# Kernel tuning notes

Measured on AMD Instinct MI355X. Metric: run time of the kernel, lower is better.

The kernel has to match this reference:

```python
import jax, jax.numpy as jnp
import numpy as np

B, S, D = 2, 2048, 640
H, DH = 8, 80  # heads, dim_head
SCALE = DH ** -0.5


def setup_inputs() -> dict:
    key = jax.random.key(0)
    ks = jax.random.split(key, 7)
    std = D ** -0.5
    return {
        "x": jax.random.normal(ks[0], (B, S, D), jnp.float32),
        "encoder_hidden_states": jax.random.normal(ks[1], (B, S, D), jnp.float32),
        # Linear weights stored as [in, out] so application is x @ W
        "Wq": jax.random.normal(ks[2], (D, H * DH), jnp.float32) * std,
        "Wk": jax.random.normal(ks[3], (D, H * DH), jnp.float32) * std,
        "Wv": jax.random.normal(ks[4], (D, H * DH), jnp.float32) * std,
        "Wo": jax.random.normal(ks[5], (H * DH, D), jnp.float32) * std,
        "bo": jax.random.normal(ks[6], (D,), jnp.float32) * 0.01,
    }


def reference(x, encoder_hidden_states, Wq, Wk, Wv, Wo, bo):
    # projections (to_q/to_k/to_v have bias=False)
    q = x @ Wq                      # [B, S, H*DH]
    k = encoder_hidden_states @ Wk  # [B, S, H*DH]
    v = encoder_hidden_states @ Wv  # [B, S, H*DH]

    def split_heads(t):
        b, s, _ = t.shape
        return t.reshape(b, s, H, DH).transpose(0, 2, 1, 3)  # [B, H, S, DH]

    q, k, v = split_heads(q), split_heads(k), split_heads(v)

    # the torch loop over bh-chunks computes plain softmax attention; same math fused
    scores = jnp.einsum("bhid,bhjd->bhij", q, k) * SCALE  # [B, H, Sq, Skv]
    attn = jax.nn.softmax(scores, axis=-1)
    out = jnp.einsum("bhij,bhjd->bhid", attn, v)          # [B, H, Sq, DH]

    out = out.transpose(0, 2, 1, 3).reshape(x.shape[0], x.shape[1], H * DH)
    return out @ Wo + bo  # to_out[0]; Dropout(p=0) is identity
```

## Files before the change

### kernel.cpp

```cpp
#include <hip/hip_runtime.h>
#include <hip/hip_bf16.h>

typedef __bf16 v4bf __attribute__((ext_vector_type(4)));
typedef __bf16 v8bf __attribute__((ext_vector_type(8)));
typedef float  v4f  __attribute__((ext_vector_type(4)));

namespace {
constexpr int Bb  = 2;
constexpr int Ss  = 2048;
constexpr int Dd  = 640;
constexpr int Hh  = 8;
constexpr int DHh = 80;
constexpr int Mm  = Bb * Ss;
constexpr float kQScale = 0.11180339887498949f * 1.4426950408889634f;

__device__ __forceinline__ float4 ld4(const float* p) {
  return *reinterpret_cast<const float4*>(p);
}

__device__ __forceinline__ v8bf pack8(float4 f0, float4 f1) {
  v8bf p;
  p[0]=(__bf16)f0.x; p[1]=(__bf16)f0.y; p[2]=(__bf16)f0.z; p[3]=(__bf16)f0.w;
  p[4]=(__bf16)f1.x; p[5]=(__bf16)f1.y; p[6]=(__bf16)f1.z; p[7]=(__bf16)f1.w;
  return p;
}

__device__ __forceinline__ float exp2_hw(float x) {
  float r;
  asm("v_exp_f32 %0, %1" : "=v"(r) : "v"(x));
  return r;
}
}

__global__ __launch_bounds__(256)
void wtrans_kernel(const float* __restrict__ Wq, const float* __restrict__ Wk,
                   const float* __restrict__ Wv, const float* __restrict__ Wo,
                   __bf16* __restrict__ Wtq, __bf16* __restrict__ Wtk,
                   __bf16* __restrict__ Wtv, __bf16* __restrict__ Wto) {
  const int z = blockIdx.z;
  const float* W = (z == 0) ? Wq : (z == 1) ? Wk : (z == 2) ? Wv : Wo;
  __bf16* Wt = (z == 0) ? Wtq : (z == 1) ? Wtk : (z == 2) ? Wtv : Wto;
  const int k0 = blockIdx.y * 32, n0 = blockIdx.x * 32;
  __shared__ float t[32][33];
  const int tid = threadIdx.x;
  {
    int kr = tid >> 3, c4 = (tid & 7) * 4;
    float4 f = ld4(W + (size_t)(k0 + kr) * Dd + n0 + c4);
    t[kr][c4 + 0] = f.x; t[kr][c4 + 1] = f.y;
    t[kr][c4 + 2] = f.z; t[kr][c4 + 3] = f.w;
  }
  __syncthreads();
  {
    int nr = tid >> 3, kc = (tid & 7) * 4;
    v4bf p;
#pragma unroll
    for (int u = 0; u < 4; ++u) p[u] = (__bf16)t[kc + u][nr];
    *reinterpret_cast<v4bf*>(&Wt[(size_t)(n0 + nr) * Dd + k0 + kc]) = p;
  }
}

__device__ __forceinline__ void gemm_core_db(const float* __restrict__ Af,
                                             const __bf16* __restrict__ Bt,
                                             __bf16* As, __bf16* Bs, int m0,
                                             int n0, int rh, int ch,
                                             v4f acc[4][4]) {
  constexpr int BUF = 128 * 40;
  constexpr int NKB = Dd / 32;
  const int tid = threadIdx.x;
  const int lane = tid & 63;
  const int quad = lane >> 4, l15 = lane & 15;
  const int lr = tid >> 1;
  const int lk = (tid & 1) * 16;
  const __bf16* Bg = Bt + (size_t)(n0 + lr) * Dd + lk;

#pragma unroll
  for (int i = 0; i < 4; ++i)
#pragma unroll
    for (int j = 0; j < 4; ++j) acc[i][j] = (v4f){0.f, 0.f, 0.f, 0.f};

  v8bf a0, a1, b0, b1;
  {
    const float* ap = Af + (size_t)(m0 + lr) * Dd + lk;
    a0 = pack8(ld4(ap), ld4(ap + 4));
    a1 = pack8(ld4(ap + 8), ld4(ap + 12));
  }
  b0 = *reinterpret_cast<const v8bf*>(Bg);
  b1 = *reinterpret_cast<const v8bf*>(Bg + 8);
  *reinterpret_cast<v8bf*>(&As[lr * 40 + lk])     = a0;
  *reinterpret_cast<v8bf*>(&As[lr * 40 + lk + 8]) = a1;
  *reinterpret_cast<v8bf*>(&Bs[lr * 40 + lk])     = b0;
  *reinterpret_cast<v8bf*>(&Bs[lr * 40 + lk + 8]) = b1;

  for (int it = 0; it < NKB; ++it) {
    if (it + 1 < NKB) {
      const int kb = (it + 1) * 32;
      const float* ap = Af + (size_t)(m0 + lr) * Dd + kb + lk;
      a0 = pack8(ld4(ap), ld4(ap + 4));
      a1 = pack8(ld4(ap + 8), ld4(ap + 12));
      b0 = *reinterpret_cast<const v8bf*>(Bg + kb);
      b1 = *reinterpret_cast<const v8bf*>(Bg + kb + 8);
    }
    __syncthreads();
    const int cur = (it & 1) * BUF, nxt = BUF - cur;
    v8bf af[4], bv[4];
#pragma unroll
    for (int i = 0; i < 4; ++i)
      af[i] = *reinterpret_cast<const v8bf*>(
          &As[cur + (rh + i * 16 + l15) * 40 + quad * 8]);
#pragma unroll
    for (int j = 0; j < 4; ++j)
      bv[j] = *reinterpret_cast<const v8bf*>(
          &Bs[cur + (ch + j * 16 + l15) * 40 + quad * 8]);
#pragma unroll
    for (int i = 0; i < 4; ++i)
#pragma unroll
      for (int j = 0; j < 4; ++j)
        acc[i][j] = __builtin_amdgcn_mfma_f32_16x16x32_bf16(af[i], bv[j],
                                                            acc[i][j], 0, 0, 0);
    if (it + 1 < NKB) {
      *reinterpret_cast<v8bf*>(&As[nxt + lr * 40 + lk])     = a0;
      *reinterpret_cast<v8bf*>(&As[nxt + lr * 40 + lk + 8]) = a1;
      *reinterpret_cast<v8bf*>(&Bs[nxt + lr * 40 + lk])     = b0;
      *reinterpret_cast<v8bf*>(&Bs[nxt + lr * 40 + lk + 8]) = b1;
    }
  }
}

__global__ __launch_bounds__(256)
void gemm_qkv_mfma(const float* __restrict__ x, const float* __restrict__ ehs,
                   const __bf16* __restrict__ Wtq,
                   const __bf16* __restrict__ Wtk,
                   const __bf16* __restrict__ Wtv, __bf16* __restrict__ qb,
                   __bf16* __restrict__ kbuf, __bf16* __restrict__ vb) {
  const int id = blockIdx.x;
  int z, mi, ni;
  if (id < 160) {
    int chunk = id / 40, r = id % 40;
    z = 0;
    mi = chunk * 8 + (r & 7);
    ni = r >> 3;
  } else {
    int id2 = id - 160;
    int chunk = id2 / 80, r = id2 % 80;
    int j = r >> 3;
    mi = chunk * 8 + (r & 7);
    ni = j % 5;
    z = 1 + j / 5;
  }
  const int m0 = mi * 128, n0 = ni * 128;

  const float* A = (z == 0) ? x : ehs;
  const __bf16* Bt = (z == 0) ? Wtq : (z == 1) ? Wtk : Wtv;
  __bf16* C = (z == 0) ? qb : (z == 1) ? kbuf : vb;
  const float scale = (z == 0) ? kQScale : 1.0f;

  __shared__ __bf16 As[2 * 128 * 40];
  __shared__ __bf16 Bs[2 * 128 * 40];
  const int tid = threadIdx.x;
  const int w = tid >> 6, lane = tid & 63;
  const int quad = lane >> 4, l15 = lane & 15;
  const int rh = (w >> 1) * 64, ch = (w & 1) * 64;
  v4f acc[4][4];
  gemm_core_db(A, Bt, As, Bs, m0, n0, rh, ch, acc);

  if (z == 2) {
#pragma unroll
    for (int i = 0; i < 4; ++i)
#pragma unroll
      for (int j = 0; j < 4; ++j) {
        int m = m0 + rh + i * 16 + quad * 4;
        int n = n0 + ch + j * 16 + l15;
        int hh = n / DHh, d = n % DHh;
        int bb = m >> 11, tok = m & 2047;
        int tb = tok >> 5, t = tok & 31;
        v4bf pk;
#pragma unroll
        for (int r = 0; r < 4; ++r) pk[r] = (__bf16)acc[i][j][r];
        *reinterpret_cast<v4bf*>(
            &C[((((size_t)bb * Hh + hh) * (Ss / 32) + tb) * DHh + d) * 32 +
               t]) = pk;
      }
  } else {
#pragma unroll
    for (int i = 0; i < 4; ++i)
#pragma unroll
      for (int j = 0; j < 4; ++j) {
        int m = m0 + rh + i * 16 + quad * 4;
        int n = n0 + ch + j * 16 + l15;
        int hh = n / DHh, d = n % DHh;
        int bb = m >> 11, tok = m & 2047;
        __bf16* base = &C[(((size_t)bb * Hh + hh) * Ss + tok) * DHh + d];
#pragma unroll
        for (int r = 0; r < 4; ++r)
          base[(size_t)r * DHh] = (__bf16)(acc[i][j][r] * scale);
      }
  }
}

__global__ __launch_bounds__(256)
void gemm_out_mfma(const __bf16* __restrict__ A, const __bf16* __restrict__ Bt,
                   const float* __restrict__ bias, float* __restrict__ out) {
  constexpr int BUF = 64 * 40;
  constexpr int NKB = Dd / 32;
  __shared__ __bf16 As[2 * BUF];
  __shared__ __bf16 Bs[2 * BUF];
  const int tid = threadIdx.x;
  const int w = tid >> 6, lane = tid & 63;
  const int quad = lane >> 4, l15 = lane & 15;
  const int m0 = blockIdx.y * 64, n0 = blockIdx.x * 64;
  const int rh = (w >> 1) * 32, ch = (w & 1) * 32;
  const int lr = tid >> 2, lk = (tid & 3) * 8;
  const __bf16* Ag = A + (size_t)(m0 + lr) * Dd + lk;
  const __bf16* Bg = Bt + (size_t)(n0 + lr) * Dd + lk;

  v4f acc[2][2];
#pragma unroll
  for (int i = 0; i < 2; ++i)
#pragma unroll
    for (int j = 0; j < 2; ++j) acc[i][j] = (v4f){0.f, 0.f, 0.f, 0.f};

  v8bf a0, b0;
  a0 = *reinterpret_cast<const v8bf*>(Ag);
  b0 = *reinterpret_cast<const v8bf*>(Bg);
  *reinterpret_cast<v8bf*>(&As[lr * 40 + lk]) = a0;
  *reinterpret_cast<v8bf*>(&Bs[lr * 40 + lk]) = b0;

  for (int it = 0; it < NKB; ++it) {
    if (it + 1 < NKB) {
      const int kb = (it + 1) * 32;
      a0 = *reinterpret_cast<const v8bf*>(Ag + kb);
      b0 = *reinterpret_cast<const v8bf*>(Bg + kb);
    }
    __syncthreads();
    const int cur = (it & 1) * BUF, nxt = BUF - cur;
    v8bf af[2], bv[2];
#pragma unroll
    for (int i = 0; i < 2; ++i)
      af[i] = *reinterpret_cast<const v8bf*>(
          &As[cur + (rh + i * 16 + l15) * 40 + quad * 8]);
#pragma unroll
    for (int j = 0; j < 2; ++j)
      bv[j] = *reinterpret_cast<const v8bf*>(
          &Bs[cur + (ch + j * 16 + l15) * 40 + quad * 8]);
#pragma unroll
    for (int i = 0; i < 2; ++i)
#pragma unroll
      for (int j = 0; j < 2; ++j)
        acc[i][j] = __builtin_amdgcn_mfma_f32_16x16x32_bf16(af[i], bv[j],
                                                            acc[i][j], 0, 0, 0);
    if (it + 1 < NKB) {
      *reinterpret_cast<v8bf*>(&As[nxt + lr * 40 + lk]) = a0;
      *reinterpret_cast<v8bf*>(&Bs[nxt + lr * 40 + lk]) = b0;
    }
  }

#pragma unroll
  for (int i = 0; i < 2; ++i)
#pragma unroll
    for (int j = 0; j < 2; ++j) {
      int m = m0 + rh + i * 16 + quad * 4;
      int n = n0 + ch + j * 16 + l15;
      float bn = bias[n];
#pragma unroll
      for (int r = 0; r < 4; ++r)
        out[(size_t)(m + r) * Dd + n] = acc[i][j][r] + bn;
    }
}

__global__ __launch_bounds__(256, 2)
void attn_mfma_kernel(const __bf16* __restrict__ q,
                      const __bf16* __restrict__ k,
                      const __bf16* __restrict__ vtg, __bf16* __restrict__ o) {
  constexpr int QT = 64;
  constexpr int KT = 32;
  constexpr int KW = Ss / 4;
  constexpr int NIT = KW / KT;
  constexpr int LV = 40;
  constexpr int PS = QT * LV;
  constexpr int LM = 100;

  __shared__ __align__(16) float smem_f[2 * QT * LM];

  const int bh = blockIdx.x;
  const int b = bh >> 3, h = bh & 7;
  const int q0 = blockIdx.y * QT;
  const int tid = threadIdx.x;
  const int w = tid >> 6;
  const int lane = tid & 63;
  const int quad = lane >> 4;
  const int l15 = lane & 15;

  __bf16* psw = reinterpret_cast<__bf16*>(smem_f) + w * PS;

  const __bf16* qg  = q + ((size_t)(b * Hh + h) * Ss + q0) * DHh;
  const __bf16* kgb = k + (size_t)(b * Hh + h) * Ss * DHh;
  const __bf16* vgb = vtg + (size_t)(b * Hh + h) * Ss * DHh;

  v8bf qf[4][3];
#pragma unroll
  for (int qt = 0; qt < 4; ++qt)
#pragma unroll
    for (int s = 0; s < 3; ++s) {
      if (s == 2 && quad >= 2) {
        qf[qt][s] = (v8bf){};
      } else {
        qf[qt][s] = *reinterpret_cast<const v8bf*>(
            qg + (size_t)(qt * 16 + l15) * DHh + s * 32 + quad * 8);
      }
    }

  v8bf av5 = {};
  if (l15 == 0) {
#pragma unroll
    for (int e = 0; e < 8; ++e) av5[e] = (__bf16)1.f;
  }

  v8bf kc[3][2];
#pragma unroll
  for (int s = 0; s < 3; ++s)
#pragma unroll
    for (int h16 = 0; h16 < 2; ++h16) {
      v8bf t = {};
      if (!(s == 2 && quad >= 2))
        t = *reinterpret_cast<const v8bf*>(
            kgb + (size_t)(w * KW + h16 * 16 + l15) * DHh + s * 32 + quad * 8);
      kc[s][h16] = t;
    }

  v4f Oacc[4][6];
#pragma unroll
  for (int qt = 0; qt < 4; ++qt)
#pragma unroll
    for (int mt = 0; mt < 6; ++mt) Oacc[qt][mt] = (v4f){0.f, 0.f, 0.f, 0.f};

  v8bf vf[5];
  for (int it = 0; it < NIT; ++it) {
    if (it > 0) {
      const __bf16* vg = vgb + (size_t)(w * 16 + (it - 1)) * (KT * DHh);
#pragma unroll
      for (int mt = 0; mt < 5; ++mt)
        vf[mt] = *reinterpret_cast<const v8bf*>(vg + (mt * 16 + l15) * 32 +
                                                quad * 8);
    }

    v4f sacc[4][2];
#pragma unroll
    for (int qt = 0; qt < 4; ++qt) {
      sacc[qt][0] = (v4f){0.f, 0.f, 0.f, 0.f};
      sacc[qt][1] = (v4f){0.f, 0.f, 0.f, 0.f};
    }
    __builtin_amdgcn_s_setprio(1);
#pragma unroll
    for (int s = 0; s < 3; ++s) {
#pragma unroll
      for (int qt = 0; qt < 4; ++qt) {
        sacc[qt][0] = __builtin_amdgcn_mfma_f32_16x16x32_bf16(
            kc[s][0], qf[qt][s], sacc[qt][0], 0, 0, 0);
        sacc[qt][1] = __builtin_amdgcn_mfma_f32_16x16x32_bf16(
            kc[s][1], qf[qt][s], sacc[qt][1], 0, 0, 0);
      }
    }

    v8bf kn[3][2];
    if (it + 1 < NIT) {
#pragma unroll
      for (int s = 0; s < 3; ++s)
#pragma unroll
        for (int h16 = 0; h16 < 2; ++h16) {
          v8bf t = {};
          if (!(s == 2 && quad >= 2))
            t = *reinterpret_cast<const v8bf*>(
                kgb + (size_t)(w * KW + (it + 1) * KT + h16 * 16 + l15) * DHh +
                s * 32 + quad * 8);
          kn[s][h16] = t;
        }
    }

    if (it > 0) {
      v8bf bp[4];
#pragma unroll
      for (int qt = 0; qt < 4; ++qt)
        bp[qt] = *reinterpret_cast<const v8bf*>(
            &psw[(qt * 16 + l15) * LV + quad * 8]);
#pragma unroll
      for (int mt = 0; mt < 5; ++mt)
#pragma unroll
        for (int qt = 0; qt < 4; ++qt)
          Oacc[qt][mt] = __builtin_amdgcn_mfma_f32_16x16x32_bf16(
              vf[mt], bp[qt], Oacc[qt][mt], 0, 0, 0);
#pragma unroll
      for (int qt = 0; qt < 4; ++qt)
        Oacc[qt][5] = __builtin_amdgcn_mfma_f32_16x16x32_bf16(
            av5, bp[qt], Oacc[qt][5], 0, 0, 0);
    }
    __builtin_amdgcn_s_setprio(0);

#pragma unroll
    for (int qt = 0; qt < 4; ++qt)
#pragma unroll
      for (int mt = 0; mt < 2; ++mt) {
        v4bf pk;
#pragma unroll
        for (int r = 0; r < 4; ++r)
          pk[r] = (__bf16)exp2_hw(sacc[qt][mt][r]);
        *reinterpret_cast<v4bf*>(
            &psw[(qt * 16 + l15) * LV + mt * 16 + quad * 4]) = pk;
      }

    if (it + 1 < NIT) {
#pragma unroll
      for (int s = 0; s < 3; ++s)
#pragma unroll
        for (int h16 = 0; h16 < 2; ++h16) kc[s][h16] = kn[s][h16];
    }
  }

  {
    const __bf16* vg = vgb + (size_t)(w * 16 + (NIT - 1)) * (KT * DHh);
#pragma unroll
    for (int mt = 0; mt < 5; ++mt)
      vf[mt] = *reinterpret_cast<const v8bf*>(vg + (mt * 16 + l15) * 32 +
                                              quad * 8);
    v8bf bp[4];
#pragma unroll
    for (int qt = 0; qt < 4; ++qt)
      bp[qt] = *reinterpret_cast<const v8bf*>(
          &psw[(qt * 16 + l15) * LV + quad * 8]);
    __builtin_amdgcn_s_setprio(1);
#pragma unroll
    for (int mt = 0; mt < 5; ++mt)
#pragma unroll
      for (int qt = 0; qt < 4; ++qt)
        Oacc[qt][mt] = __builtin_amdgcn_mfma_f32_16x16x32_bf16(
            vf[mt], bp[qt], Oacc[qt][mt], 0, 0, 0);
#pragma unroll
    for (int qt = 0; qt < 4; ++qt)
      Oacc[qt][5] = __builtin_amdgcn_mfma_f32_16x16x32_bf16(
          av5, bp[qt], Oacc[qt][5], 0, 0, 0);
    __builtin_amdgcn_s_setprio(0);
  }

  __syncthreads();
  float* mrg = smem_f;
  if (w >= 2) {
    float* base = mrg + (w - 2) * (QT * LM);
#pragma unroll
    for (int qt = 0; qt < 4; ++qt)
#pragma unroll
      for (int mt = 0; mt < 6; ++mt)
        *reinterpret_cast<v4f*>(
            &base[(qt * 16 + l15) * LM + mt * 16 + quad * 4]) = Oacc[qt][mt];
  }
  __syncthreads();
  if (w < 2) {
    const float* base = mrg + w * (QT * LM);
#pragma unroll
    for (int qt = 0; qt < 4; ++qt)
#pragma unroll
      for (int mt = 0; mt < 6; ++mt)
        Oacc[qt][mt] += *reinterpret_cast<const v4f*>(
            &base[(qt * 16 + l15) * LM + mt * 16 + quad * 4]);
  }
  __syncthreads();
  if (w == 1) {
#pragma unroll
    for (int qt = 0; qt < 4; ++qt)
#pragma unroll
      for (int mt = 0; mt < 6; ++mt)
        *reinterpret_cast<v4f*>(
            &mrg[(qt * 16 + l15) * LM + mt * 16 + quad * 4]) = Oacc[qt][mt];
  }
  __syncthreads();
  if (w == 0) {
#pragma unroll
    for (int qt = 0; qt < 4; ++qt)
#pragma unroll
      for (int mt = 0; mt < 6; ++mt)
        Oacc[qt][mt] += *reinterpret_cast<const v4f*>(
            &mrg[(qt * 16 + l15) * LM + mt * 16 + quad * 4]);
#pragma unroll
    for (int qt = 0; qt < 4; ++qt) {
      float lsum = __shfl(Oacc[qt][5][0], l15);
      float inv = 1.f / lsum;
      __bf16* og =
          o + (size_t)(b * Ss + q0 + qt * 16 + l15) * Dd + h * DHh;
#pragma unroll
      for (int mt = 0; mt < 5; ++mt) {
        v4bf pk;
#pragma unroll
        for (int r = 0; r < 4; ++r) pk[r] = (__bf16)(Oacc[qt][mt][r] * inv);
        *reinterpret_cast<v4bf*>(&og[mt * 16 + quad * 4]) = pk;
      }
    }
  }
}

extern "C" void kernel_launch(void* const* d_in, const int* in_sizes, int n_in,
                              void* d_out, int out_size, void* d_ws,
                              size_t ws_size, hipStream_t stream) {
  const float* x   = (const float*)d_in[0];
  const float* ehs = (const float*)d_in[1];
  const float* Wq  = (const float*)d_in[2];
  const float* Wk  = (const float*)d_in[3];
  const float* Wv  = (const float*)d_in[4];
  const float* Wo  = (const float*)d_in[5];
  const float* bo  = (const float*)d_in[6];
  float* out = (float*)d_out;

  __bf16* qb  = (__bf16*)d_ws;
  __bf16* kb  = qb + (size_t)Mm * Dd;
  __bf16* vb  = kb + (size_t)Mm * Dd;
  __bf16* ab  = vb + (size_t)Mm * Dd;
  __bf16* Wtq = ab + (size_t)Mm * Dd;
  __bf16* Wtk = Wtq + (size_t)Dd * Dd;
  __bf16* Wtv = Wtk + (size_t)Dd * Dd;
  __bf16* Wto = Wtv + (size_t)Dd * Dd;

  wtrans_kernel<<<dim3(Dd / 32, Dd / 32, 4), 256, 0, stream>>>(
      Wq, Wk, Wv, Wo, Wtq, Wtk, Wtv, Wto);
  gemm_qkv_mfma<<<dim3(480), 256, 0, stream>>>(
      x, ehs, Wtq, Wtk, Wtv, qb, kb, vb);
  attn_mfma_kernel<<<dim3(Bb * Hh, Ss / 64), 256, 0, stream>>>(qb, kb, vb, ab);
  gemm_out_mfma<<<dim3(Dd / 64, Mm / 64), 256, 0, stream>>>(ab, Wto, bo,
                                                            out);
}
```

Before: 139.4 us.

## Split attention KV range across eight waves with tree reduction merge

The attention block grows from 256 to 512 threads, so each of 8 waves handles one eighth of the key/value sequence instead of one quarter. The partial output accumulators are then combined with a multi-stage pairwise reduction through shared memory, using two buffers. The aim is more in-flight waves and shorter per-wave loops to hide latency. The launch bound is raised to (512, 4), which tightens the per-thread register budget against large accumulator arrays and may cause spills. The merge also adds more barriers.

```diff
diff --git a/kernel.cpp b/kernel.cpp
--- a/kernel.cpp
+++ b/kernel.cpp
@@ -267,13 +267,13 @@
     }
 }
 
-__global__ __launch_bounds__(256, 2)
+__global__ __launch_bounds__(512, 4)
 void attn_mfma_kernel(const __bf16* __restrict__ q,
                       const __bf16* __restrict__ k,
                       const __bf16* __restrict__ vtg, __bf16* __restrict__ o) {
   constexpr int QT = 64;
   constexpr int KT = 32;
-  constexpr int KW = Ss / 4;
+  constexpr int KW = Ss / 8;
   constexpr int NIT = KW / KT;
   constexpr int LV = 40;
   constexpr int PS = QT * LV;
@@ -336,7 +336,7 @@
   v8bf vf[5];
   for (int it = 0; it < NIT; ++it) {
     if (it > 0) {
-      const __bf16* vg = vgb + (size_t)(w * 16 + (it - 1)) * (KT * DHh);
+      const __bf16* vg = vgb + (size_t)(w * NIT + (it - 1)) * (KT * DHh);
 #pragma unroll
       for (int mt = 0; mt < 5; ++mt)
         vf[mt] = *reinterpret_cast<const v8bf*>(vg + (mt * 16 + l15) * 32 +
@@ -416,7 +416,7 @@
   }
 
   {
-    const __bf16* vg = vgb + (size_t)(w * 16 + (NIT - 1)) * (KT * DHh);
+    const __bf16* vg = vgb + (size_t)(w * NIT + (NIT - 1)) * (KT * DHh);
 #pragma unroll
     for (int mt = 0; mt < 5; ++mt)
       vf[mt] = *reinterpret_cast<const v8bf*>(vg + (mt * 16 + l15) * 32 +
@@ -440,44 +440,36 @@
     __builtin_amdgcn_s_setprio(0);
   }
 
-  __syncthreads();
-  float* mrg = smem_f;
-  if (w >= 2) {
-    float* base = mrg + (w - 2) * (QT * LM);
-#pragma unroll
-    for (int qt = 0; qt < 4; ++qt)
-#pragma unroll
-      for (int mt = 0; mt < 6; ++mt)
-        *reinterpret_cast<v4f*>(
-            &base[(qt * 16 + l15) * LM + mt * 16 + quad * 4]) = Oacc[qt][mt];
-  }
-  __syncthreads();
-  if (w < 2) {
-    const float* base = mrg + w * (QT * LM);
-#pragma unroll
-    for (int qt = 0; qt < 4; ++qt)
-#pragma unroll
-      for (int mt = 0; mt < 6; ++mt)
-        Oacc[qt][mt] += *reinterpret_cast<const v4f*>(
-            &base[(qt * 16 + l15) * LM + mt * 16 + quad * 4]);
-  }
-  __syncthreads();
-  if (w == 1) {
-#pragma unroll
-    for (int qt = 0; qt < 4; ++qt)
-#pragma unroll
-      for (int mt = 0; mt < 6; ++mt)
-        *reinterpret_cast<v4f*>(
-            &mrg[(qt * 16 + l15) * LM + mt * 16 + quad * 4]) = Oacc[qt][mt];
-  }
+  float* s0 = smem_f;
+  float* s1 = smem_f + QT * LM;
+#define MERGE_STORE(dst)                                                  \
+  _Pragma("unroll") for (int qt = 0; qt < 4; ++qt)                        \
+      _Pragma("unroll") for (int mt = 0; mt < 6; ++mt)                    \
+          *reinterpret_cast<v4f*>(                                        \
+              &(dst)[(qt * 16 + l15) * LM + mt * 16 + quad * 4]) =        \
+              Oacc[qt][mt];
+#define MERGE_ADD(src)                                                    \
+  _Pragma("unroll") for (int qt = 0; qt < 4; ++qt)                        \
+      _Pragma("unroll") for (int mt = 0; mt < 6; ++mt)                    \
+          Oacc[qt][mt] += *reinterpret_cast<const v4f*>(                  \
+              &(src)[(qt * 16 + l15) * LM + mt * 16 + quad * 4]);
+  __syncthreads();
+  if (w == 1) { MERGE_STORE(s0); } else if (w == 3) { MERGE_STORE(s1); }
+  __syncthreads();
+  if (w == 0) { MERGE_ADD(s0); } else if (w == 2) { MERGE_ADD(s1); }
+  __syncthreads();
+  if (w == 5) { MERGE_STORE(s0); } else if (w == 7) { MERGE_STORE(s1); }
+  __syncthreads();
+  if (w == 4) { MERGE_ADD(s0); } else if (w == 6) { MERGE_ADD(s1); }
+  __syncthreads();
+  if (w == 2) { MERGE_STORE(s0); } else if (w == 6) { MERGE_STORE(s1); }
+  __syncthreads();
+  if (w == 0) { MERGE_ADD(s0); } else if (w == 4) { MERGE_ADD(s1); }
+  __syncthreads();
+  if (w == 4) { MERGE_STORE(s0); }
   __syncthreads();
   if (w == 0) {
-#pragma unroll
-    for (int qt = 0; qt < 4; ++qt)
-#pragma unroll
-      for (int mt = 0; mt < 6; ++mt)
-        Oacc[qt][mt] += *reinterpret_cast<const v4f*>(
-            &mrg[(qt * 16 + l15) * LM + mt * 16 + quad * 4]);
+    MERGE_ADD(s0);
 #pragma unroll
     for (int qt = 0; qt < 4; ++qt) {
       float lsum = __shfl(Oacc[qt][5][0], l15);
@@ -493,6 +485,8 @@
       }
     }
   }
+#undef MERGE_STORE
+#undef MERGE_ADD
 }
 
 extern "C" void kernel_launch(void* const* d_in, const int* in_sizes, int n_in,
@@ -520,7 +514,7 @@
       Wq, Wk, Wv, Wo, Wtq, Wtk, Wtv, Wto);
   gemm_qkv_mfma<<<dim3(480), 256, 0, stream>>>(
       x, ehs, Wtq, Wtk, Wtv, qb, kb, vb);
-  attn_mfma_kernel<<<dim3(Bb * Hh, Ss / 64), 256, 0, stream>>>(qb, kb, vb, ab);
+  attn_mfma_kernel<<<dim3(Bb * Hh, Ss / 64), 512, 0, stream>>>(qb, kb, vb, ab);
   gemm_out_mfma<<<dim3(Dd / 64, Mm / 64), 256, 0, stream>>>(ab, Wto, bo,
                                                             out);
 }
```

Measured after the change: 363.5 us. +160.8%, slower.
